# Performance work log

Hardware: AMD Instinct MI355X
Metric: run time of the kernel (lower is better)

## Reference

```python
import jax, jax.numpy as jnp
import numpy as np

C = 256
DF = 8
CQK = C // DF  # 32


def setup_inputs() -> dict:
    key = jax.random.key(0)
    ks = jax.random.split(key, 7)
    s = 0.02
    x = jax.random.normal(ks[0], (4, C, 64, 64), dtype=jnp.float32)
    Wq = jax.random.normal(ks[1], (CQK, C), dtype=jnp.float32) * s
    bq = jnp.zeros((CQK,), dtype=jnp.float32)
    Wk = jax.random.normal(ks[2], (CQK, C), dtype=jnp.float32) * s
    bk = jnp.zeros((CQK,), dtype=jnp.float32)
    Wv = jax.random.normal(ks[3], (C, C), dtype=jnp.float32) * s
    bv = jnp.zeros((C,), dtype=jnp.float32)
    gamma = jnp.ones((1,), dtype=jnp.float32)  # nonzero so output is nontrivial
    return {"x": x, "Wq": Wq, "bq": bq, "Wk": Wk, "bk": bk, "Wv": Wv, "bv": bv, "gamma": gamma}


def reference(x, Wq, bq, Wk, bk, Wv, bv, gamma):
    B, Cc, H, W = x.shape
    # flatten spatial: [B, N, C] with N = H*W
    xf = x.reshape(B, Cc, H * W).transpose(0, 2, 1)
    # 1x1 convs == per-pixel linear projections
    q = jnp.einsum('bnc,dc->bnd', xf, Wq) + bq        # [B, N, Cqk]
    k = jnp.einsum('bnc,dc->bnd', xf, Wk) + bk        # [B, N, Cqk]
    v = jnp.einsum('bnc,dc->bnd', xf, Wv) + bv        # [B, N, C]
    energy = jnp.einsum('bnd,bmd->bnm', q, k)          # [B, N, N], no scale (as in source)
    attn = jax.nn.softmax(energy, axis=-1)
    out = jnp.einsum('bnm,bmc->bnc', attn, v)          # [B, N, C]
    out = out.transpose(0, 2, 1).reshape(B, Cc, H, W)
    return gamma[0] * out
```

## Files before the change

kernel.cpp:

```cpp
#include <hip/hip_runtime.h>
#include <hip/hip_bf16.h>


typedef __attribute__((ext_vector_type(8))) short s8v;
typedef __attribute__((ext_vector_type(4))) float f4v;

#define NPIX 4096
#define CIN 256
#define DQK 32

#if __has_builtin(__builtin_amdgcn_exp2f)
#define EXP2(x) __builtin_amdgcn_exp2f(x)
#else
#define EXP2(x) exp2f(x)
#endif

static __device__ __forceinline__ unsigned short f2bf(float f) {
    union { float f; unsigned int u; } v; v.f = f;
    unsigned int r = v.u + 0x7FFF + ((v.u >> 16) & 1);
    return (unsigned short)(r >> 16);
}
static __device__ __forceinline__ unsigned int fbits(float f) {
    union { float f; unsigned int u; } v; v.f = f; return v.u;
}

__global__ void wcast_kernel(const float* __restrict__ Wq, const float* __restrict__ bq,
                             const float* __restrict__ Wk, const float* __restrict__ bk,
                             const float* __restrict__ Wv, const float* __restrict__ bv,
                             unsigned short* __restrict__ Wall, float* __restrict__ ball) {
    int row = blockIdx.x;
    int t = threadIdx.x;
    const float* src; const float* bsrc;
    if (row < 32)       { src = Wq + row * 256;        bsrc = bq + row; }
    else if (row < 64)  { src = Wk + (row - 32) * 256; bsrc = bk + (row - 32); }
    else                { src = Wv + (row - 64) * 256; bsrc = bv + (row - 64); }
    Wall[row * 256 + t] = f2bf(src[t]);
    if (t == 0) ball[row] = bsrc[0];
}

__global__ void tcast_kernel(const float* __restrict__ x, unsigned short* __restrict__ xT) {
    __shared__ unsigned short tile[64][65];
    int bidx = blockIdx.x;
    int b    = bidx >> 8;
    int cblk = (bidx >> 6) & 3;
    int nblk = bidx & 63;
    int t = threadIdx.x;
    int c0 = cblk * 64, n0 = nblk * 64;
    const float* xb = x + (size_t)b * CIN * NPIX;
    #pragma unroll
    for (int p = 0; p < 4; p++) {
        int cl = p * 16 + (t >> 4);
        int nl = (t & 15) * 4;
        float4 v = *(const float4*)(xb + (size_t)(c0 + cl) * NPIX + n0 + nl);
        tile[cl][nl + 0] = f2bf(v.x);
        tile[cl][nl + 1] = f2bf(v.y);
        tile[cl][nl + 2] = f2bf(v.z);
        tile[cl][nl + 3] = f2bf(v.w);
    }
    __syncthreads();
    unsigned short* xTb = xT + (size_t)b * NPIX * CIN;
    #pragma unroll
    for (int p = 0; p < 4; p++) {
        int nl = p * 16 + (t >> 4);
        int cl = (t & 15) * 4;
        ushort4 wv;
        wv.x = tile[cl + 0][nl];
        wv.y = tile[cl + 1][nl];
        wv.z = tile[cl + 2][nl];
        wv.w = tile[cl + 3][nl];
        *(ushort4*)(xTb + (size_t)(n0 + nl) * CIN + c0 + cl) = wv;
    }
}

__global__ __launch_bounds__(256)
void proj_kernel(const unsigned short* __restrict__ xT,
                 const unsigned short* __restrict__ Wall,
                 const float* __restrict__ ball,
                 unsigned short* __restrict__ Q,
                 unsigned short* __restrict__ Kp,
                 unsigned short* __restrict__ Vt) {
    int idx  = blockIdx.x;
    int b    = (idx & 7) >> 1;
    int nblk = ((idx >> 3) << 1) | (idx & 1);
    int w    = threadIdx.x >> 6;
    int lane = threadIdx.x & 63;
    int l16 = lane & 15, quad = lane >> 4;
    int n0 = nblk * 64 + w * 16;

    const unsigned short* brow = xT + (size_t)(b * NPIX + n0 + l16) * CIN + quad * 8;
    s8v bfr[8];
    #pragma unroll
    for (int kk = 0; kk < 8; kk++) bfr[kk] = *(const s8v*)(brow + kk * 32);

    #pragma unroll
    for (int p = 0; p < 10; p++) {
        const unsigned short* w0 = Wall + (size_t)(2 * p * 16 + l16) * CIN + quad * 8;
        const unsigned short* w1 = w0 + 16 * CIN;
        f4v a0 = {0.f, 0.f, 0.f, 0.f}, a1 = {0.f, 0.f, 0.f, 0.f};
        if (p < 2) {
            #pragma unroll
            for (int kk = 0; kk < 8; kk++) {
                a0 = __builtin_amdgcn_mfma_f32_16x16x32_bf16(bfr[kk], *(const s8v*)(w0 + kk * 32), a0, 0, 0, 0);
                a1 = __builtin_amdgcn_mfma_f32_16x16x32_bf16(bfr[kk], *(const s8v*)(w1 + kk * 32), a1, 0, 0, 0);
            }
        } else {
            #pragma unroll
            for (int kk = 0; kk < 8; kk++) {
                a0 = __builtin_amdgcn_mfma_f32_16x16x32_bf16(*(const s8v*)(w0 + kk * 32), bfr[kk], a0, 0, 0, 0);
                a1 = __builtin_amdgcn_mfma_f32_16x16x32_bf16(*(const s8v*)(w1 + kk * 32), bfr[kk], a1, 0, 0, 0);
            }
        }
        #pragma unroll
        for (int half = 0; half < 2; half++) {
            int ob = 2 * p + half;
            f4v acc = half ? a1 : a0;
            if (ob < 2) {
                int oc = ob * 16 + l16;
                float bias = ball[oc];
                #pragma unroll
                for (int r = 0; r < 4; r++) {
                    int n = n0 + quad * 4 + r;
                    Q[(size_t)(b * NPIX + n) * DQK + oc] =
                        f2bf((acc[r] + bias) * 1.44269504f);
                }
            } else if (ob < 4) {
                int oc = (ob - 2) * 16 + l16;
                float bias = ball[32 + oc];
                #pragma unroll
                for (int r = 0; r < 4; r++) {
                    int n = n0 + quad * 4 + r;
                    int pn = (n & ~31) | (((n >> 2) & 1) << 4) | (((n >> 3) & 3) << 2) | (n & 3);
                    Kp[(size_t)(b * NPIX + pn) * DQK + oc] = f2bf(acc[r] + bias);
                }
            } else {
                int n = n0 + l16;
                #pragma unroll
                for (int r = 0; r < 4; r++) {
                    int ch = (ob - 4) * 16 + quad * 4 + r;
                    Vt[((size_t)b * CIN + ch) * NPIX + n] = f2bf(acc[r] + ball[64 + ch]);
                }
            }
        }
    }
}

#define ATTN_STEP(BUF, KC0, KC1, VC, KN0, KN1, VN, NKV_NEXT)                    \
    {                                                                           \
        KN0 = *(const s8v*)(kbase + (NKV_NEXT) * DQK);                          \
        KN1 = *(const s8v*)(kbase + ((NKV_NEXT) + 16) * DQK);                   \
        _Pragma("unroll")                                                       \
        for (int ct = 0; ct < 4; ct++)                                          \
            VN[ct] = *(const s8v*)(vbase + ct * 16 * NPIX + (NKV_NEXT));        \
        f4v s0 = {0.f, 0.f, 0.f, 0.f}, s1 = {0.f, 0.f, 0.f, 0.f};               \
        s0 = __builtin_amdgcn_mfma_f32_16x16x32_bf16(KC0, qf, s0, 0, 0, 0);     \
        s1 = __builtin_amdgcn_mfma_f32_16x16x32_bf16(KC1, qf, s1, 0, 0, 0);     \
        float p00 = EXP2(s0[0]), p01 = EXP2(s0[1]);                             \
        float p02 = EXP2(s0[2]), p03 = EXP2(s0[3]);                             \
        float p10 = EXP2(s1[0]), p11 = EXP2(s1[1]);                             \
        float p12 = EXP2(s1[2]), p13 = EXP2(s1[3]);                             \
        lsum += ((p00 + p01) + (p02 + p03)) + ((p10 + p11) + (p12 + p13));      \
        union { uint4 u; s8v v; } pp;                                           \
        pp.u.x = __builtin_amdgcn_perm(fbits(p01), fbits(p00), 0x07060302);     \
        pp.u.y = __builtin_amdgcn_perm(fbits(p03), fbits(p02), 0x07060302);     \
        pp.u.z = __builtin_amdgcn_perm(fbits(p11), fbits(p10), 0x07060302);     \
        pp.u.w = __builtin_amdgcn_perm(fbits(p13), fbits(p12), 0x07060302);     \
        *(uint4*)(Pme + (BUF) * 1024) = pp.u;                                   \
        __asm__ __volatile__("s_waitcnt lgkmcnt(0)\n\ts_barrier" ::: "memory"); \
        s8v pa[4];                                                              \
        _Pragma("unroll")                                                       \
        for (int rt = 0; rt < 4; rt++) {                                        \
            if (rt == cj) pa[rt] = pp.v;                                        \
            else          pa[rt] = *(const s8v*)(Pkh + (BUF) * 1024 + rt * 256);\
        }                                                                       \
        _Pragma("unroll")                                                       \
        for (int ct = 0; ct < 4; ct++)                                          \
            _Pragma("unroll")                                                   \
            for (int rt = 0; rt < 4; rt++)                                      \
                O[rt][ct] = __builtin_amdgcn_mfma_f32_16x16x32_bf16(VC[ct], pa[rt], O[rt][ct], 0, 0, 0); \
    }

__global__ __launch_bounds__(512)
void attn_kernel(const unsigned short* __restrict__ Q,
                 const unsigned short* __restrict__ Kp,
                 const unsigned short* __restrict__ Vt,
                 const float* __restrict__ gamma,
                 float* __restrict__ out) {
    __shared__ __align__(16) char smem[70144];

    int idx = blockIdx.x;
    int b      = (idx & 7) >> 1;
    int rowblk = ((idx >> 3) << 1) | (idx & 1);

    int lane = threadIdx.x & 63;
    int w    = threadIdx.x >> 6;
    int l16 = lane & 15, quad = lane >> 4;
    int kh = w >> 2;
    int cj = w & 3;

    const unsigned short* Kb = Kp + (size_t)b * NPIX * DQK;
    const unsigned short* Vb = Vt + (size_t)b * CIN * NPIX;

    int rowbase = rowblk * 64;
    const s8v qf = *(const s8v*)(Q + (size_t)(b * NPIX + rowbase + cj * 16 + l16) * DQK + quad * 8);

    const unsigned short* kbase = Kb + (32 * kh + l16) * DQK + quad * 8;
    const unsigned short* vbase = Vb + (size_t)(cj * 64 + l16) * NPIX + 32 * kh + quad * 8;

    int lswz = l16 * 16 + ((quad ^ (l16 & 3)) << 2);
    unsigned int* Pkh = (unsigned int*)smem + kh * 2048 + lswz;
    unsigned int* Pme = Pkh + cj * 256;

    f4v O[4][4];
    #pragma unroll
    for (int rt = 0; rt < 4; rt++)
        #pragma unroll
        for (int ct = 0; ct < 4; ct++) O[rt][ct] = (f4v){0.f, 0.f, 0.f, 0.f};
    float lsum = 0.f;

    s8v Kc0, Kc1, Kn0, Kn1, Vc[4], Vn[4];
    Kc0 = *(const s8v*)(kbase);
    Kc1 = *(const s8v*)(kbase + 16 * DQK);
    #pragma unroll
    for (int ct = 0; ct < 4; ct++)
        Vc[ct] = *(const s8v*)(vbase + ct * 16 * NPIX);

    for (int kv2 = 0; kv2 < NPIX; kv2 += 128) {
        ATTN_STEP(0, Kc0, Kc1, Vc, Kn0, Kn1, Vn, kv2 + 64);
        ATTN_STEP(1, Kn0, Kn1, Vn, Kc0, Kc1, Vc, (kv2 + 128) & (NPIX - 1));
    }

    lsum += __shfl_xor(lsum, 16);
    lsum += __shfl_xor(lsum, 32);

    __syncthreads();

    float (*ldsO)[64][68] = (float (*)[64][68])smem;
    float* ldsL = (float*)(smem + 69632);

    if (quad == 0) ldsL[kh * 64 + cj * 16 + l16] = lsum;
    if (kh == 1) {
        #pragma unroll
        for (int rt = 0; rt < 4; rt++)
            #pragma unroll
            for (int ct = 0; ct < 4; ct++)
                *(f4v*)&ldsO[cj][lane][(rt * 4 + ct) * 4] = O[rt][ct];
    }
    __syncthreads();

    if (kh == 0) {
        float g = gamma[0];
        float rinv[4];
        #pragma unroll
        for (int rt = 0; rt < 4; rt++)
            rinv[rt] = g / (ldsL[rt * 16 + l16] + ldsL[64 + rt * 16 + l16]);
        #pragma unroll
        for (int rt = 0; rt < 4; rt++) {
            #pragma unroll
            for (int ct = 0; ct < 4; ct++) {
                f4v o2 = *(const f4v*)&ldsO[cj][lane][(rt * 4 + ct) * 4];
                #pragma unroll
                for (int r = 0; r < 4; r++) {
                    int ch = cj * 64 + ct * 16 + quad * 4 + r;
                    out[((size_t)b * CIN + ch) * NPIX + rowbase + rt * 16 + l16] =
                        (O[rt][ct][r] + o2[r]) * rinv[rt];
                }
            }
        }
    }
}

extern "C" void kernel_launch(void* const* d_in, const int* in_sizes, int n_in,
                              void* d_out, int out_size, void* d_ws, size_t ws_size,
                              hipStream_t stream) {
    const float* x     = (const float*)d_in[0];
    const float* Wq    = (const float*)d_in[1];
    const float* bq    = (const float*)d_in[2];
    const float* Wk    = (const float*)d_in[3];
    const float* bk    = (const float*)d_in[4];
    const float* Wv    = (const float*)d_in[5];
    const float* bv    = (const float*)d_in[6];
    const float* gamma = (const float*)d_in[7];
    float* out = (float*)d_out;

    char* p = (char*)d_ws;
    unsigned short* xT   = (unsigned short*)p; p += (size_t)4 * NPIX * CIN * 2;
    unsigned short* Qb   = (unsigned short*)p; p += (size_t)4 * NPIX * DQK * 2;
    unsigned short* Kb   = (unsigned short*)p; p += (size_t)4 * NPIX * DQK * 2;
    unsigned short* Vt   = (unsigned short*)p; p += (size_t)4 * CIN * NPIX * 2;
    unsigned short* Wall = (unsigned short*)p; p += (size_t)320 * 256 * 2;
    float*          ball = (float*)p;          p += (size_t)320 * 4;

    wcast_kernel<<<320, 256, 0, stream>>>(Wq, bq, Wk, bk, Wv, bv, Wall, ball);
    tcast_kernel<<<1024, 256, 0, stream>>>(x, xT);
    proj_kernel<<<256, 256, 0, stream>>>(xT, Wall, ball, Qb, Kb, Vt);
    attn_kernel<<<256, 512, 0, stream>>>(Qb, Kb, Vt, gamma, out);
}
```

Before: 185.0 us.

## Software-pipeline attention loop so P·V of previous step overlaps QK of next

Restructures the attention main loop so each step reads the previous step's shared P tile and runs its P·V MFMAs while computing the current step's QK scores and exp. The current P tile is written to a double buffer and the barrier moves to the end of the step, taking it off the critical path between the QK and PV phases. A prologue and epilogue handle the first and last steps, and the LDS swizzle changes to an XOR over 8 slots to reduce bank conflicts. The trade-off is more live registers and more complex indexing, which could raise register pressure.

```diff
diff --git a/kernel.cpp b/kernel.cpp
--- a/kernel.cpp
+++ b/kernel.cpp
@@ -13,6 +13,12 @@
 #define EXP2(x) __builtin_amdgcn_exp2f(x)
 #else
 #define EXP2(x) exp2f(x)
+#endif
+
+#if __has_builtin(__builtin_amdgcn_s_waitcnt)
+#define LGKM0_BARRIER() { __builtin_amdgcn_s_waitcnt(0xC07F); __builtin_amdgcn_s_barrier(); }
+#else
+#define LGKM0_BARRIER() { __asm__ __volatile__("s_waitcnt lgkmcnt(0)\n\ts_barrier" ::: "memory"); }
 #endif
 
 static __device__ __forceinline__ unsigned short f2bf(float f) {
@@ -144,13 +150,19 @@
     }
 }
 
-#define ATTN_STEP(BUF, KC0, KC1, VC, KN0, KN1, VN, NKV_NEXT)                    \
+#define ATTN_STEP(S, WB, KC0, KC1, VC, KN0, KN1, VN)                            \
     {                                                                           \
-        KN0 = *(const s8v*)(kbase + (NKV_NEXT) * DQK);                          \
-        KN1 = *(const s8v*)(kbase + ((NKV_NEXT) + 16) * DQK);                   \
+        const int kvn = ((S) + 1) & 63;                                         \
+        KN0 = *(const s8v*)(kbase + (size_t)(kvn * 64) * DQK);                  \
+        KN1 = *(const s8v*)(kbase + (size_t)(kvn * 64 + 16) * DQK);             \
         _Pragma("unroll")                                                       \
         for (int ct = 0; ct < 4; ct++)                                          \
-            VN[ct] = *(const s8v*)(vbase + ct * 16 * NPIX + (NKV_NEXT));        \
+            VN[ct] = *(const s8v*)(vbase + (size_t)ct * 16 * NPIX + (S) * 64);  \
+        const unsigned int* rb = smemw + khw + (1 - (WB)) * 1024;               \
+        s8v pa0 = (cj == 0) ? ppv : *(const s8v*)(rb + rdo0);                   \
+        s8v pa1 = (cj == 1) ? ppv : *(const s8v*)(rb + rdo1);                   \
+        s8v pa2 = (cj == 2) ? ppv : *(const s8v*)(rb + rdo2);                   \
+        s8v pa3 = (cj == 3) ? ppv : *(const s8v*)(rb + rdo3);                   \
         f4v s0 = {0.f, 0.f, 0.f, 0.f}, s1 = {0.f, 0.f, 0.f, 0.f};               \
         s0 = __builtin_amdgcn_mfma_f32_16x16x32_bf16(KC0, qf, s0, 0, 0, 0);     \
         s1 = __builtin_amdgcn_mfma_f32_16x16x32_bf16(KC1, qf, s1, 0, 0, 0);     \
@@ -164,19 +176,16 @@
         pp.u.y = __builtin_amdgcn_perm(fbits(p03), fbits(p02), 0x07060302);     \
         pp.u.z = __builtin_amdgcn_perm(fbits(p11), fbits(p10), 0x07060302);     \
         pp.u.w = __builtin_amdgcn_perm(fbits(p13), fbits(p12), 0x07060302);     \
-        *(uint4*)(Pme + (BUF) * 1024) = pp.u;                                   \
-        __asm__ __volatile__("s_waitcnt lgkmcnt(0)\n\ts_barrier" ::: "memory"); \
-        s8v pa[4];                                                              \
+        *(uint4*)(smemw + khw + (WB) * 1024 + wro) = pp.u;                      \
         _Pragma("unroll")                                                       \
-        for (int rt = 0; rt < 4; rt++) {                                        \
-            if (rt == cj) pa[rt] = pp.v;                                        \
-            else          pa[rt] = *(const s8v*)(Pkh + (BUF) * 1024 + rt * 256);\
+        for (int ct = 0; ct < 4; ct++) {                                        \
+            O[0][ct] = __builtin_amdgcn_mfma_f32_16x16x32_bf16(VC[ct], pa0, O[0][ct], 0, 0, 0); \
+            O[1][ct] = __builtin_amdgcn_mfma_f32_16x16x32_bf16(VC[ct], pa1, O[1][ct], 0, 0, 0); \
+            O[2][ct] = __builtin_amdgcn_mfma_f32_16x16x32_bf16(VC[ct], pa2, O[2][ct], 0, 0, 0); \
+            O[3][ct] = __builtin_amdgcn_mfma_f32_16x16x32_bf16(VC[ct], pa3, O[3][ct], 0, 0, 0); \
         }                                                                       \
-        _Pragma("unroll")                                                       \
-        for (int ct = 0; ct < 4; ct++)                                          \
-            _Pragma("unroll")                                                   \
-            for (int rt = 0; rt < 4; rt++)                                      \
-                O[rt][ct] = __builtin_amdgcn_mfma_f32_16x16x32_bf16(VC[ct], pa[rt], O[rt][ct], 0, 0, 0); \
+        LGKM0_BARRIER();                                                        \
+        ppv = pp.v;                                                             \
     }
 
 __global__ __launch_bounds__(512)
@@ -186,6 +195,7 @@
                  const float* __restrict__ gamma,
                  float* __restrict__ out) {
     __shared__ __align__(16) char smem[70144];
+    unsigned int* smemw = (unsigned int*)smem;
 
     int idx = blockIdx.x;
     int b      = (idx & 7) >> 1;
@@ -206,9 +216,12 @@
     const unsigned short* kbase = Kb + (32 * kh + l16) * DQK + quad * 8;
     const unsigned short* vbase = Vb + (size_t)(cj * 64 + l16) * NPIX + 32 * kh + quad * 8;
 
-    int lswz = l16 * 16 + ((quad ^ (l16 & 3)) << 2);
-    unsigned int* Pkh = (unsigned int*)smem + kh * 2048 + lswz;
-    unsigned int* Pme = Pkh + cj * 256;
+    const int khw  = kh * 2048;
+    const int wro  = l16 * 64 + (((cj * 4 + quad) ^ (l16 & 7)) << 2);
+    const int rdo0 = l16 * 64 + (((0 * 4 + quad) ^ (l16 & 7)) << 2);
+    const int rdo1 = l16 * 64 + (((1 * 4 + quad) ^ (l16 & 7)) << 2);
+    const int rdo2 = l16 * 64 + (((2 * 4 + quad) ^ (l16 & 7)) << 2);
+    const int rdo3 = l16 * 64 + (((3 * 4 + quad) ^ (l16 & 7)) << 2);
 
     f4v O[4][4];
     #pragma unroll
@@ -216,17 +229,56 @@
         #pragma unroll
         for (int ct = 0; ct < 4; ct++) O[rt][ct] = (f4v){0.f, 0.f, 0.f, 0.f};
     float lsum = 0.f;
+    s8v ppv;
 
     s8v Kc0, Kc1, Kn0, Kn1, Vc[4], Vn[4];
     Kc0 = *(const s8v*)(kbase);
     Kc1 = *(const s8v*)(kbase + 16 * DQK);
-    #pragma unroll
-    for (int ct = 0; ct < 4; ct++)
-        Vc[ct] = *(const s8v*)(vbase + ct * 16 * NPIX);
-
-    for (int kv2 = 0; kv2 < NPIX; kv2 += 128) {
-        ATTN_STEP(0, Kc0, Kc1, Vc, Kn0, Kn1, Vn, kv2 + 64);
-        ATTN_STEP(1, Kn0, Kn1, Vn, Kc0, Kc1, Vc, (kv2 + 128) & (NPIX - 1));
+
+    {
+        Kn0 = *(const s8v*)(kbase + (size_t)64 * DQK);
+        Kn1 = *(const s8v*)(kbase + (size_t)80 * DQK);
+        #pragma unroll
+        for (int ct = 0; ct < 4; ct++)
+            Vc[ct] = *(const s8v*)(vbase + (size_t)ct * 16 * NPIX);
+        f4v s0 = {0.f, 0.f, 0.f, 0.f}, s1 = {0.f, 0.f, 0.f, 0.f};
+        s0 = __builtin_amdgcn_mfma_f32_16x16x32_bf16(Kc0, qf, s0, 0, 0, 0);
+        s1 = __builtin_amdgcn_mfma_f32_16x16x32_bf16(Kc1, qf, s1, 0, 0, 0);
+        float p00 = EXP2(s0[0]), p01 = EXP2(s0[1]);
+        float p02 = EXP2(s0[2]), p03 = EXP2(s0[3]);
+        float p10 = EXP2(s1[0]), p11 = EXP2(s1[1]);
+        float p12 = EXP2(s1[2]), p13 = EXP2(s1[3]);
+        lsum += ((p00 + p01) + (p02 + p03)) + ((p10 + p11) + (p12 + p13));
+        union { uint4 u; s8v v; } pp;
+        pp.u.x = __builtin_amdgcn_perm(fbits(p01), fbits(p00), 0x07060302);
+        pp.u.y = __builtin_amdgcn_perm(fbits(p03), fbits(p02), 0x07060302);
+        pp.u.z = __builtin_amdgcn_perm(fbits(p11), fbits(p10), 0x07060302);
+        pp.u.w = __builtin_amdgcn_perm(fbits(p13), fbits(p12), 0x07060302);
+        *(uint4*)(smemw + khw + 0 * 1024 + wro) = pp.u;
+        LGKM0_BARRIER();
+        ppv = pp.v;
+    }
+
+    for (int p = 0; p < 31; p++) {
+        int s1i = 2 * p + 1;
+        ATTN_STEP(s1i,     1, Kn0, Kn1, Vc, Kc0, Kc1, Vn);
+        ATTN_STEP(s1i + 1, 0, Kc0, Kc1, Vn, Kn0, Kn1, Vc);
+    }
+    ATTN_STEP(63, 1, Kn0, Kn1, Vc, Kc0, Kc1, Vn);
+
+    {
+        const unsigned int* rb = smemw + khw + 1024;
+        s8v pa0 = (cj == 0) ? ppv : *(const s8v*)(rb + rdo0);
+        s8v pa1 = (cj == 1) ? ppv : *(const s8v*)(rb + rdo1);
+        s8v pa2 = (cj == 2) ? ppv : *(const s8v*)(rb + rdo2);
+        s8v pa3 = (cj == 3) ? ppv : *(const s8v*)(rb + rdo3);
+        #pragma unroll
+        for (int ct = 0; ct < 4; ct++) {
+            O[0][ct] = __builtin_amdgcn_mfma_f32_16x16x32_bf16(Vn[ct], pa0, O[0][ct], 0, 0, 0);
+            O[1][ct] = __builtin_amdgcn_mfma_f32_16x16x32_bf16(Vn[ct], pa1, O[1][ct], 0, 0, 0);
+            O[2][ct] = __builtin_amdgcn_mfma_f32_16x16x32_bf16(Vn[ct], pa2, O[2][ct], 0, 0, 0);
+            O[3][ct] = __builtin_amdgcn_mfma_f32_16x16x32_bf16(Vn[ct], pa3, O[3][ct], 0, 0, 0);
+        }
     }
 
     lsum += __shfl_xor(lsum, 16);
```

Result: no change. 182.7 us (-1.2%).
